# Optimization experiments

Measured on AMD Instinct MI355X. Metric: run time of the kernel, lower is better.

The kernel has to match this reference:

```python
import jax, jax.numpy as jnp
import numpy as np

NUM_HEADS = 8
N_POINTS = 9
OFFSET_SCALE = 4.0


def bilinear_sample(fmap_flat, xy, H, W):
    """fmap_flat: (BH, H*W, C) row-major spatial; xy: (BH, S, 2) pixel coords (x, y).
    grid_sample(mode='bilinear', padding_mode='zeros', align_corners=True) equivalent.
    Returns (BH, S, C)."""
    x, y = xy[..., 0], xy[..., 1]
    x0 = jnp.floor(x); y0 = jnp.floor(y)
    x1 = x0 + 1.0;    y1 = y0 + 1.0
    wx1 = x - x0; wx0 = 1.0 - wx1
    wy1 = y - y0; wy0 = 1.0 - wy1

    def corner(xi, yi, wgt):
        valid = (xi >= 0) & (xi <= W - 1) & (yi >= 0) & (yi <= H - 1)
        xi_c = jnp.clip(xi, 0, W - 1).astype(jnp.int32)
        yi_c = jnp.clip(yi, 0, H - 1).astype(jnp.int32)
        idx = yi_c * W + xi_c                                   # (BH, S)
        vals = jnp.take_along_axis(fmap_flat, idx[..., None], axis=1)  # (BH, S, C)
        return vals * (wgt * valid.astype(fmap_flat.dtype))[..., None]

    return (corner(x0, y0, wx0 * wy0) + corner(x1, y0, wx1 * wy0)
            + corner(x0, y1, wx0 * wy1) + corner(x1, y1, wx1 * wy1))


def setup_inputs() -> dict:
    key = jax.random.key(0)
    ks = jax.random.split(key, 10)
    B, N, D = 4, 6400, 256
    Hh, P = NUM_HEADS, N_POINTS
    s = 0.02
    return {
        "x":    jax.random.normal(ks[0], (B, N, D), dtype=jnp.float32),
        "Wq":   jax.random.normal(ks[1], (D, D), dtype=jnp.float32) * s,
        "bq":   jnp.zeros((D,), jnp.float32),
        "Woff": jax.random.normal(ks[2], (Hh * P * 2, D), dtype=jnp.float32) * s,
        "boff": jax.random.normal(ks[3], (Hh * P * 2,), dtype=jnp.float32) * s,
        "Wkv":  jax.random.normal(ks[4], (2 * D, D), dtype=jnp.float32) * s,
        "bkv":  jnp.zeros((2 * D,), jnp.float32),
        "Wout": jax.random.normal(ks[5], (D, D), dtype=jnp.float32) * s,
        "bout": jnp.zeros((D,), jnp.float32),
        "h": 40,
        "w": 160,
    }


def reference(x, Wq, bq, Woff, boff, Wkv, bkv, Wout, bout, h, w):
    B, N, D = x.shape
    H, P = NUM_HEADS, N_POINTS
    hd = D // H

    # queries: (B, H, N, hd)
    q = (x @ Wq.T + bq).reshape(B, N, H, hd).transpose(0, 2, 1, 3)

    # per-query per-head offsets in pixels: (B, N, H, P, 2) (dx, dy)
    offsets = jnp.tanh(x @ Woff.T + boff).reshape(B, N, H, P, 2) * OFFSET_SCALE

    # K/V feature maps via 1x1 conv == per-token linear; split heads, flat spatial
    kv = x @ Wkv.T + bkv                     # (B, N, 2D)
    k = kv[..., :D]
    v = kv[..., D:]
    k_flat = k.reshape(B, N, H, hd).transpose(0, 2, 1, 3).reshape(B * H, N, hd)
    v_flat = v.reshape(B, N, H, hd).transpose(0, 2, 1, 3).reshape(B * H, N, hd)

    # base pixel grid (x, y), row-major over (h, w)
    ys, xs = jnp.meshgrid(jnp.arange(h, dtype=x.dtype), jnp.arange(w, dtype=x.dtype), indexing="ij")
    base_xy = jnp.stack([xs, ys], axis=-1).reshape(N, 2)

    # sampling locations: (B, N, H, P, 2) -> (B*H, N*P, 2)
    sample_xy = base_xy[None, :, None, None, :] + offsets
    sample_xy = sample_xy.transpose(0, 2, 1, 3, 4).reshape(B * H, N * P, 2)

    sampled_k = bilinear_sample(k_flat, sample_xy, h, w).reshape(B, H, N, P, hd)
    sampled_v = bilinear_sample(v_flat, sample_xy, h, w).reshape(B, H, N, P, hd)

    logits = jnp.einsum("bhnd,bhnpd->bhnp", q, sampled_k) * (hd ** -0.5)
    attn = jax.nn.softmax(logits, axis=-1)
    out = jnp.einsum("bhnp,bhnpd->bhnd", attn, sampled_v)   # (B, H, N, hd)
    out = out.transpose(0, 2, 1, 3).reshape(B, N, D)
    return out @ Wout.T + bout
```

## Files before the change

### kernel.cpp

```cpp
#include <hip/hip_runtime.h>
#include <math.h>

#define BSZ    4
#define NTOK   6400
#define DMODEL 256
#define NHEAD  8
#define HDIM   32
#define NPTS   9
#define HSP    40
#define WSP    160
#define KDIM   256
#define MTOT   (BSZ*NTOK)

typedef short  short8  __attribute__((ext_vector_type(8)));
typedef float  floatx4 __attribute__((ext_vector_type(4)));
typedef float  f32x2   __attribute__((ext_vector_type(2)));

__device__ __forceinline__ ushort f2bf(float f) {
    uint u = __float_as_uint(f);
    u = (u + 0x7FFFu + ((u >> 16) & 1u)) >> 16;
    return (ushort)u;
}

__device__ __forceinline__ void unpack8v(uint4 u, f32x2* f) {
    f[0].x = __uint_as_float(u.x << 16); f[0].y = __uint_as_float(u.x & 0xFFFF0000u);
    f[1].x = __uint_as_float(u.y << 16); f[1].y = __uint_as_float(u.y & 0xFFFF0000u);
    f[2].x = __uint_as_float(u.z << 16); f[2].y = __uint_as_float(u.z & 0xFFFF0000u);
    f[3].x = __uint_as_float(u.w << 16); f[3].y = __uint_as_float(u.w & 0xFFFF0000u);
}

__device__ __forceinline__ float dot8(uint4 u, const f32x2* q2) {
    f32x2 a; a.x = 0.f; a.y = 0.f;
    f32x2 t;
    t.x = __uint_as_float(u.x << 16); t.y = __uint_as_float(u.x & 0xFFFF0000u);
    a += t * q2[0];
    t.x = __uint_as_float(u.y << 16); t.y = __uint_as_float(u.y & 0xFFFF0000u);
    a += t * q2[1];
    t.x = __uint_as_float(u.z << 16); t.y = __uint_as_float(u.z & 0xFFFF0000u);
    a += t * q2[2];
    t.x = __uint_as_float(u.w << 16); t.y = __uint_as_float(u.w & 0xFFFF0000u);
    a += t * q2[3];
    return a.x + a.y;
}

#define AS1C(p) ((const __attribute__((address_space(1))) void*)(p))
#define AS3(p)  ((__attribute__((address_space(3))) void*)(p))

__global__ __launch_bounds__(256) void cast_all(
    const float* __restrict__ x,   const float* __restrict__ Wq,
    const float* __restrict__ Woff,const float* __restrict__ Wkv,
    const float* __restrict__ Wout,
    ushort* __restrict__ xb, ushort* __restrict__ wf, ushort* __restrict__ woutb)
{
    const int bid = blockIdx.x;
    if (bid >= 6500 && bid < 6528) {
        const int i = (bid - 6500) * 1024 + threadIdx.x * 4;
        ushort4 z; z.x = 0; z.y = 0; z.z = 0; z.w = 0;
        *(ushort4*)(wf + 400 * 256 + i) = z;
        return;
    }
    const float* src; ushort* dst; int base;
    if      (bid < 6400) { src = x;    dst = xb;              base = bid; }
    else if (bid < 6464) { src = Wq;   dst = wf;              base = bid - 6400; }
    else if (bid < 6500) { src = Woff; dst = wf + 256 * 256;  base = bid - 6464; }
    else if (bid < 6656) { src = Wkv;  dst = wf + 512 * 256;  base = bid - 6528; }
    else                 { src = Wout; dst = woutb;           base = bid - 6656; }
    const int i = base * 1024 + threadIdx.x * 4;
    float4 v = *(const float4*)(src + i);
    ushort4 o;
    o.x = f2bf(v.x); o.y = f2bf(v.y); o.z = f2bf(v.z); o.w = f2bf(v.w);
    *(ushort4*)(dst + i) = o;
}

__global__ __launch_bounds__(256) void gemm_fused(
    const ushort* __restrict__ Xb,
    const ushort* __restrict__ Wf,
    const float* __restrict__ bq, const float* __restrict__ boff,
    const float* __restrict__ bkv,
    ushort* __restrict__ qb, float* __restrict__ off,
    ushort* __restrict__ kfb, ushort* __restrict__ vfb)
{
    __shared__ ushort As[128 * 32];
    __shared__ ushort Bs[128 * 32];

    const int tid = threadIdx.x;
    const int block_m = blockIdx.y * 128;
    const int block_n = blockIdx.x * 128;
    const int wave = tid >> 6, lane = tid & 63;
    const int wm = (wave >> 1) * 64, wn = (wave & 1) * 64;
    const int l15 = lane & 15, quad = lane >> 4;

    const int srow = wave * 32 + (lane >> 2);
    const int scol = (lane & 3) * 8;

    const ushort* gA0 = Xb + (size_t)(block_m + srow) * KDIM + scol;
    const ushort* gA1 = gA0 + 16 * KDIM;
    const ushort* gB0 = Wf + (size_t)(block_n + srow) * KDIM + scol;
    const ushort* gB1 = gB0 + 16 * KDIM;

    ushort* lA0 = &As[(wave * 32) * 32];
    ushort* lA1 = &As[(wave * 32 + 16) * 32];
    ushort* lB0 = &Bs[(wave * 32) * 32];
    ushort* lB1 = &Bs[(wave * 32 + 16) * 32];

    floatx4 acc[4][4];
    #pragma unroll
    for (int i = 0; i < 4; ++i)
        #pragma unroll
        for (int j = 0; j < 4; ++j) {
            acc[i][j][0] = 0.f; acc[i][j][1] = 0.f;
            acc[i][j][2] = 0.f; acc[i][j][3] = 0.f;
        }

    for (int k0 = 0; k0 < KDIM; k0 += 32) {
        __builtin_amdgcn_global_load_lds(AS1C(gA0 + k0), AS3(lA0), 16, 0, 0);
        __builtin_amdgcn_global_load_lds(AS1C(gA1 + k0), AS3(lA1), 16, 0, 0);
        __builtin_amdgcn_global_load_lds(AS1C(gB0 + k0), AS3(lB0), 16, 0, 0);
        __builtin_amdgcn_global_load_lds(AS1C(gB1 + k0), AS3(lB1), 16, 0, 0);
        __syncthreads();

        short8 af[4], bfr[4];
        #pragma unroll
        for (int f = 0; f < 4; ++f) {
            af[f]  = *(const short8*)&As[(wm + f * 16 + l15) * 32 + quad * 8];
            bfr[f] = *(const short8*)&Bs[(wn + f * 16 + l15) * 32 + quad * 8];
        }
        #pragma unroll
        for (int fm = 0; fm < 4; ++fm)
            #pragma unroll
            for (int fn = 0; fn < 4; ++fn)
                acc[fm][fn] = __builtin_amdgcn_mfma_f32_16x16x32_bf16(
                    af[fm], bfr[fn], acc[fm][fn], 0, 0, 0);
        __syncthreads();
    }

    #pragma unroll
    for (int fn = 0; fn < 4; ++fn) {
        const int col = block_n + wn + fn * 16 + l15;
        float bcol;
        if      (col < 256) bcol = bq[col];
        else if (col < 400) bcol = boff[col - 256];
        else if (col < 512) bcol = 0.f;
        else                bcol = bkv[col - 512];
        #pragma unroll
        for (int fm = 0; fm < 4; ++fm) {
            #pragma unroll
            for (int r = 0; r < 4; ++r) {
                const int row = block_m + wm + fm * 16 + quad * 4 + r;
                const float val = acc[fm][fn][r] + bcol;
                if (col < 256) {
                    qb[(size_t)row * DMODEL + col] = f2bf(val);
                } else if (col < 400) {
                    off[(size_t)row * 144 + (col - 256)] = tanhf(val) * 4.0f;
                } else if (col >= 512) {
                    const int c2 = col - 512;
                    const int bb = row / NTOK, nn = row % NTOK;
                    const int hh = (c2 & 255) >> 5, cc = c2 & 31;
                    const size_t o = (((size_t)(bb * NHEAD + hh)) * NTOK + nn) * HDIM + cc;
                    if (c2 < 256) kfb[o] = f2bf(val);
                    else          vfb[o] = f2bf(val);
                }
            }
        }
    }
}

__global__ __launch_bounds__(256) void gemm_out(
    const ushort* __restrict__ Xb,
    const ushort* __restrict__ Wb,
    const float* __restrict__ bias,
    float* __restrict__ Y)
{
    __shared__ ushort As[128 * 32];
    __shared__ ushort Bs[128 * 32];

    const int tid = threadIdx.x;
    const int block_m = blockIdx.y * 128;
    const int block_n = blockIdx.x * 128;
    const int wave = tid >> 6, lane = tid & 63;
    const int wm = (wave >> 1) * 64, wn = (wave & 1) * 64;
    const int l15 = lane & 15, quad = lane >> 4;

    const int srow = wave * 32 + (lane >> 2);
    const int scol = (lane & 3) * 8;

    const ushort* gA0 = Xb + (size_t)(block_m + srow) * KDIM + scol;
    const ushort* gA1 = gA0 + 16 * KDIM;
    const ushort* gB0 = Wb + (size_t)(block_n + srow) * KDIM + scol;
    const ushort* gB1 = gB0 + 16 * KDIM;

    ushort* lA0 = &As[(wave * 32) * 32];
    ushort* lA1 = &As[(wave * 32 + 16) * 32];
    ushort* lB0 = &Bs[(wave * 32) * 32];
    ushort* lB1 = &Bs[(wave * 32 + 16) * 32];

    floatx4 acc[4][4];
    #pragma unroll
    for (int i = 0; i < 4; ++i)
        #pragma unroll
        for (int j = 0; j < 4; ++j) {
            acc[i][j][0] = 0.f; acc[i][j][1] = 0.f;
            acc[i][j][2] = 0.f; acc[i][j][3] = 0.f;
        }

    for (int k0 = 0; k0 < KDIM; k0 += 32) {
        __builtin_amdgcn_global_load_lds(AS1C(gA0 + k0), AS3(lA0), 16, 0, 0);
        __builtin_amdgcn_global_load_lds(AS1C(gA1 + k0), AS3(lA1), 16, 0, 0);
        __builtin_amdgcn_global_load_lds(AS1C(gB0 + k0), AS3(lB0), 16, 0, 0);
        __builtin_amdgcn_global_load_lds(AS1C(gB1 + k0), AS3(lB1), 16, 0, 0);
        __syncthreads();

        short8 af[4], bfr[4];
        #pragma unroll
        for (int f = 0; f < 4; ++f) {
            af[f]  = *(const short8*)&As[(wm + f * 16 + l15) * 32 + quad * 8];
            bfr[f] = *(const short8*)&Bs[(wn + f * 16 + l15) * 32 + quad * 8];
        }
        #pragma unroll
        for (int fm = 0; fm < 4; ++fm)
            #pragma unroll
            for (int fn = 0; fn < 4; ++fn)
                acc[fm][fn] = __builtin_amdgcn_mfma_f32_16x16x32_bf16(
                    af[fm], bfr[fn], acc[fm][fn], 0, 0, 0);
        __syncthreads();
    }

    #pragma unroll
    for (int fn = 0; fn < 4; ++fn) {
        const int col = block_n + wn + fn * 16 + l15;
        const float bcol = bias[col];
        #pragma unroll
        for (int fm = 0; fm < 4; ++fm) {
            #pragma unroll
            for (int r = 0; r < 4; ++r) {
                const int row = block_m + wm + fm * 16 + quad * 4 + r;
                Y[(size_t)row * DMODEL + col] = acc[fm][fn][r] + bcol;
            }
        }
    }
}

__global__ __launch_bounds__(256) void deform_attn(
    const ushort* __restrict__ qb,
    const float* __restrict__ off,
    const ushort* __restrict__ kfb,
    const ushort* __restrict__ vfb,
    ushort* __restrict__ attnb)
{
    const int lane = threadIdx.x & 63;
    const int token = blockIdx.x * 8 + (threadIdx.x >> 6) * 2 + (lane >> 5);
    const int h = (lane >> 2) & 7, lc = lane & 3;
    const int b = token / NTOK, n = token % NTOK;

    const uint4 qu = *(const uint4*)(qb + (size_t)token * DMODEL + h * HDIM + lc * 8);
    f32x2 q2[4]; unpack8v(qu, q2);

    const float* ob = off + (size_t)token * 144 + h * (NPTS * 2);
    const float bx = (float)(n % WSP), by = (float)(n / WSP);
    const ushort* kbase = kfb + (size_t)(b * NHEAD + h) * NTOK * HDIM + lc * 8;
    const ushort* vbase = vfb + (size_t)(b * NHEAD + h) * NTOK * HDIM + lc * 8;

    float m = -INFINITY, s = 0.f;
    f32x2 o2[4];
    #pragma unroll
    for (int i = 0; i < 4; ++i) { o2[i].x = 0.f; o2[i].y = 0.f; }

    #pragma unroll
    for (int g = 0; g < 3; ++g) {
        int   idx[3][4];
        float wt[3][4];
        #pragma unroll
        for (int j = 0; j < 3; ++j) {
            const int p = g * 3 + j;
            const float2 of = *(const float2*)(ob + 2 * p);
            const float sx = bx + of.x, sy = by + of.y;
            const float fx0 = floorf(sx), fy0 = floorf(sy);
            const float wx1 = sx - fx0, wx0 = 1.0f - wx1;
            const float wy1 = sy - fy0, wy0 = 1.0f - wy1;
            const int ix0 = (int)fx0, iy0 = (int)fy0;
            const int ix1 = ix0 + 1, iy1 = iy0 + 1;
            const bool vx0 = (ix0 >= 0) & (ix0 <= WSP - 1);
            const bool vx1 = (ix1 >= 0) & (ix1 <= WSP - 1);
            const bool vy0 = (iy0 >= 0) & (iy0 <= HSP - 1);
            const bool vy1 = (iy1 >= 0) & (iy1 <= HSP - 1);
            const int cx0 = min(max(ix0, 0), WSP - 1);
            const int cx1 = min(max(ix1, 0), WSP - 1);
            const int cy0 = min(max(iy0, 0), HSP - 1);
            const int cy1 = min(max(iy1, 0), HSP - 1);
            wt[j][0] = wx0 * wy0 * (float)(vx0 && vy0);
            wt[j][1] = wx1 * wy0 * (float)(vx1 && vy0);
            wt[j][2] = wx0 * wy1 * (float)(vx0 && vy1);
            wt[j][3] = wx1 * wy1 * (float)(vx1 && vy1);
            idx[j][0] = (cy0 * WSP + cx0) * HDIM;
            idx[j][1] = (cy0 * WSP + cx1) * HDIM;
            idx[j][2] = (cy1 * WSP + cx0) * HDIM;
            idx[j][3] = (cy1 * WSP + cx1) * HDIM;
        }

        float l[3];
        #pragma unroll
        for (int j = 0; j < 3; ++j) {
            const uint4 k0 = *(const uint4*)(kbase + idx[j][0]);
            const uint4 k1 = *(const uint4*)(kbase + idx[j][1]);
            const uint4 k2 = *(const uint4*)(kbase + idx[j][2]);
            const uint4 k3 = *(const uint4*)(kbase + idx[j][3]);
            float part = wt[j][0] * dot8(k0, q2) + wt[j][1] * dot8(k1, q2)
                       + wt[j][2] * dot8(k2, q2) + wt[j][3] * dot8(k3, q2);
            part += __shfl_xor(part, 1, 64);
            part += __shfl_xor(part, 2, 64);
            l[j] = part * 0.17677669529663687f;
        }

        const float m1 = fmaxf(fmaxf(fmaxf(l[0], l[1]), l[2]), m);
        const float corr = __expf(m - m1);
        const float e0 = __expf(l[0] - m1);
        const float e1 = __expf(l[1] - m1);
        const float e2 = __expf(l[2] - m1);
        s = s * corr + e0 + e1 + e2;
        m = m1;
        const float e[3] = {e0, e1, e2};

        #pragma unroll
        for (int i = 0; i < 4; ++i) o2[i] *= corr;

        #pragma unroll
        for (int j = 0; j < 3; ++j) {
            #pragma unroll
            for (int c = 0; c < 4; ++c) {
                const uint4 vu = *(const uint4*)(vbase + idx[j][c]);
                f32x2 vv[4]; unpack8v(vu, vv);
                const float ew = e[j] * wt[j][c];
                #pragma unroll
                for (int i = 0; i < 4; ++i) o2[i] += vv[i] * ew;
            }
        }
    }

    const float inv = 1.0f / s;
    uint4 ru;
    ru.x = (uint)f2bf(o2[0].x * inv) | ((uint)f2bf(o2[0].y * inv) << 16);
    ru.y = (uint)f2bf(o2[1].x * inv) | ((uint)f2bf(o2[1].y * inv) << 16);
    ru.z = (uint)f2bf(o2[2].x * inv) | ((uint)f2bf(o2[2].y * inv) << 16);
    ru.w = (uint)f2bf(o2[3].x * inv) | ((uint)f2bf(o2[3].y * inv) << 16);
    *(uint4*)(attnb + (size_t)token * DMODEL + h * HDIM + lc * 8) = ru;
}

extern "C" void kernel_launch(void* const* d_in, const int* in_sizes, int n_in,
                              void* d_out, int out_size, void* d_ws, size_t ws_size,
                              hipStream_t stream) {
    const float* x    = (const float*)d_in[0];
    const float* Wq   = (const float*)d_in[1];
    const float* bq   = (const float*)d_in[2];
    const float* Woff = (const float*)d_in[3];
    const float* boff = (const float*)d_in[4];
    const float* Wkv  = (const float*)d_in[5];
    const float* bkv  = (const float*)d_in[6];
    const float* Wout = (const float*)d_in[7];
    const float* bout = (const float*)d_in[8];

    ushort* xb    = (ushort*)d_ws;
    ushort* qb    = xb + (size_t)MTOT * DMODEL;
    float*  off   = (float*)(qb + (size_t)MTOT * DMODEL);
    ushort* kfb   = (ushort*)(off + (size_t)MTOT * 144);
    ushort* vfb   = kfb + (size_t)MTOT * DMODEL;
    ushort* wf    = vfb + (size_t)MTOT * DMODEL;
    ushort* woutb = wf + 262144;
    ushort* attnb = xb;

    cast_all<<<dim3(6720), dim3(256), 0, stream>>>(x, Wq, Woff, Wkv, Wout,
                                                   xb, wf, woutb);

    gemm_fused<<<dim3(8, 200), dim3(256), 0, stream>>>(xb, wf, bq, boff, bkv,
                                                       qb, off, kfb, vfb);

    deform_attn<<<dim3(3200), dim3(256), 0, stream>>>(qb, off, kfb, vfb, attnb);

    gemm_out<<<dim3(2, 200), dim3(256), 0, stream>>>(attnb, woutb, bout,
                                                     (float*)d_out);
}
```

Before: 217.4 us.

## Stage full-K A tile in swizzled LDS, read B from global, XCD-aware block mapping

Both GEMMs now share one templated kernel. It loads the whole 128x256 A tile into XOR-swizzled LDS once, then runs the K loop with no per-step barriers. B fragments are read directly from global memory, where the small weights should stay cached. Blocks are remapped so that consecutive blocks on the same XCD share A rows, which should improve L2 locality. The trade-offs are 64KB of LDS per block, which lowers occupancy, and uncoalesced global B loads inside the MFMA loop.

```diff
diff --git a/kernel.cpp b/kernel.cpp
--- a/kernel.cpp
+++ b/kernel.cpp
@@ -72,58 +72,64 @@
     *(ushort4*)(dst + i) = o;
 }
 
-__global__ __launch_bounds__(256) void gemm_fused(
+template <int MODE>
+__global__ __launch_bounds__(256) void gemm_fullk(
     const ushort* __restrict__ Xb,
     const ushort* __restrict__ Wf,
     const float* __restrict__ bq, const float* __restrict__ boff,
     const float* __restrict__ bkv,
     ushort* __restrict__ qb, float* __restrict__ off,
-    ushort* __restrict__ kfb, ushort* __restrict__ vfb)
+    ushort* __restrict__ kfb, ushort* __restrict__ vfb,
+    float* __restrict__ Yout)
 {
-    __shared__ ushort As[128 * 32];
-    __shared__ ushort Bs[128 * 32];
+    constexpr int NBN = (MODE == 0) ? 8 : 2;
+    __shared__ ushort As[4 * 128 * 64];
 
     const int tid = threadIdx.x;
-    const int block_m = blockIdx.y * 128;
-    const int block_n = blockIdx.x * 128;
+    const int bid = blockIdx.x;
+    const int xcd = bid & 7;
+    const int j   = bid >> 3;
+    const int block_n = (j & (NBN - 1)) * 128;
+    const int block_m = (xcd * 25 + j / NBN) * 128;
+
     const int wave = tid >> 6, lane = tid & 63;
     const int wm = (wave >> 1) * 64, wn = (wave & 1) * 64;
     const int l15 = lane & 15, quad = lane >> 4;
 
-    const int srow = wave * 32 + (lane >> 2);
-    const int scol = (lane & 3) * 8;
-
-    const ushort* gA0 = Xb + (size_t)(block_m + srow) * KDIM + scol;
-    const ushort* gA1 = gA0 + 16 * KDIM;
-    const ushort* gB0 = Wf + (size_t)(block_n + srow) * KDIM + scol;
-    const ushort* gB1 = gB0 + 16 * KDIM;
-
-    ushort* lA0 = &As[(wave * 32) * 32];
-    ushort* lA1 = &As[(wave * 32 + 16) * 32];
-    ushort* lB0 = &Bs[(wave * 32) * 32];
-    ushort* lB1 = &Bs[(wave * 32 + 16) * 32];
+    const int r8   = lane >> 3;
+    const int gsrc = (lane & 7) ^ r8;
+    #pragma unroll
+    for (int kc = 0; kc < 4; ++kc) {
+        #pragma unroll
+        for (int i = 0; i < 4; ++i) {
+            const int rl = wave * 32 + i * 8;
+            const ushort* src = Xb + (size_t)(block_m + rl + r8) * KDIM
+                                   + kc * 64 + gsrc * 8;
+            ushort* dst = As + kc * (128 * 64) + rl * 64;
+            __builtin_amdgcn_global_load_lds(AS1C(src), AS3(dst), 16, 0, 0);
+        }
+    }
+    __syncthreads();
 
     floatx4 acc[4][4];
     #pragma unroll
     for (int i = 0; i < 4; ++i)
         #pragma unroll
-        for (int j = 0; j < 4; ++j) {
-            acc[i][j][0] = 0.f; acc[i][j][1] = 0.f;
-            acc[i][j][2] = 0.f; acc[i][j][3] = 0.f;
-        }
-
-    for (int k0 = 0; k0 < KDIM; k0 += 32) {
-        __builtin_amdgcn_global_load_lds(AS1C(gA0 + k0), AS3(lA0), 16, 0, 0);
-        __builtin_amdgcn_global_load_lds(AS1C(gA1 + k0), AS3(lA1), 16, 0, 0);
-        __builtin_amdgcn_global_load_lds(AS1C(gB0 + k0), AS3(lB0), 16, 0, 0);
-        __builtin_amdgcn_global_load_lds(AS1C(gB1 + k0), AS3(lB1), 16, 0, 0);
-        __syncthreads();
-
+        for (int jj = 0; jj < 4; ++jj) {
+            acc[i][jj][0] = 0.f; acc[i][jj][1] = 0.f;
+            acc[i][jj][2] = 0.f; acc[i][jj][3] = 0.f;
+        }
+
+    #pragma unroll
+    for (int ks = 0; ks < 8; ++ks) {
         short8 af[4], bfr[4];
         #pragma unroll
         for (int f = 0; f < 4; ++f) {
-            af[f]  = *(const short8*)&As[(wm + f * 16 + l15) * 32 + quad * 8];
-            bfr[f] = *(const short8*)&Bs[(wn + f * 16 + l15) * 32 + quad * 8];
+            const int rowa = wm + f * 16 + l15;
+            const int gsw  = (((ks & 1) * 4 + quad) ^ (l15 & 7));
+            af[f]  = *(const short8*)(As + (ks >> 1) * (128 * 64) + rowa * 64 + gsw * 8);
+            bfr[f] = *(const short8*)(Wf + (size_t)(block_n + wn + f * 16 + l15) * KDIM
+                                         + ks * 32 + quad * 8);
         }
         #pragma unroll
         for (int fm = 0; fm < 4; ++fm)
@@ -131,110 +137,42 @@
             for (int fn = 0; fn < 4; ++fn)
                 acc[fm][fn] = __builtin_amdgcn_mfma_f32_16x16x32_bf16(
                     af[fm], bfr[fn], acc[fm][fn], 0, 0, 0);
-        __syncthreads();
     }
 
     #pragma unroll
     for (int fn = 0; fn < 4; ++fn) {
         const int col = block_n + wn + fn * 16 + l15;
         float bcol;
-        if      (col < 256) bcol = bq[col];
-        else if (col < 400) bcol = boff[col - 256];
-        else if (col < 512) bcol = 0.f;
-        else                bcol = bkv[col - 512];
+        if (MODE == 1) {
+            bcol = bq[col];
+        } else {
+            if      (col < 256) bcol = bq[col];
+            else if (col < 400) bcol = boff[col - 256];
+            else if (col < 512) bcol = 0.f;
+            else                bcol = bkv[col - 512];
+        }
         #pragma unroll
         for (int fm = 0; fm < 4; ++fm) {
             #pragma unroll
             for (int r = 0; r < 4; ++r) {
                 const int row = block_m + wm + fm * 16 + quad * 4 + r;
                 const float val = acc[fm][fn][r] + bcol;
-                if (col < 256) {
-                    qb[(size_t)row * DMODEL + col] = f2bf(val);
-                } else if (col < 400) {
-                    off[(size_t)row * 144 + (col - 256)] = tanhf(val) * 4.0f;
-                } else if (col >= 512) {
-                    const int c2 = col - 512;
-                    const int bb = row / NTOK, nn = row % NTOK;
-                    const int hh = (c2 & 255) >> 5, cc = c2 & 31;
-                    const size_t o = (((size_t)(bb * NHEAD + hh)) * NTOK + nn) * HDIM + cc;
-                    if (c2 < 256) kfb[o] = f2bf(val);
-                    else          vfb[o] = f2bf(val);
+                if (MODE == 1) {
+                    Yout[(size_t)row * DMODEL + col] = val;
+                } else {
+                    if (col < 256) {
+                        qb[(size_t)row * DMODEL + col] = f2bf(val);
+                    } else if (col < 400) {
+                        off[(size_t)row * 144 + (col - 256)] = tanhf(val) * 4.0f;
+                    } else if (col >= 512) {
+                        const int c2 = col - 512;
+                        const int bb = row / NTOK, nn = row % NTOK;
+                        const int hh = (c2 & 255) >> 5, cc = c2 & 31;
+                        const size_t o = (((size_t)(bb * NHEAD + hh)) * NTOK + nn) * HDIM + cc;
+                        if (c2 < 256) kfb[o] = f2bf(val);
+                        else          vfb[o] = f2bf(val);
+                    }
                 }
-            }
-        }
-    }
-}
-
-__global__ __launch_bounds__(256) void gemm_out(
-    const ushort* __restrict__ Xb,
-    const ushort* __restrict__ Wb,
-    const float* __restrict__ bias,
-    float* __restrict__ Y)
-{
-    __shared__ ushort As[128 * 32];
-    __shared__ ushort Bs[128 * 32];
-
-    const int tid = threadIdx.x;
-    const int block_m = blockIdx.y * 128;
-    const int block_n = blockIdx.x * 128;
-    const int wave = tid >> 6, lane = tid & 63;
-    const int wm = (wave >> 1) * 64, wn = (wave & 1) * 64;
-    const int l15 = lane & 15, quad = lane >> 4;
-
-    const int srow = wave * 32 + (lane >> 2);
-    const int scol = (lane & 3) * 8;
-
-    const ushort* gA0 = Xb + (size_t)(block_m + srow) * KDIM + scol;
-    const ushort* gA1 = gA0 + 16 * KDIM;
-    const ushort* gB0 = Wb + (size_t)(block_n + srow) * KDIM + scol;
-    const ushort* gB1 = gB0 + 16 * KDIM;
-
-    ushort* lA0 = &As[(wave * 32) * 32];
-    ushort* lA1 = &As[(wave * 32 + 16) * 32];
-    ushort* lB0 = &Bs[(wave * 32) * 32];
-    ushort* lB1 = &Bs[(wave * 32 + 16) * 32];
-
-    floatx4 acc[4][4];
-    #pragma unroll
-    for (int i = 0; i < 4; ++i)
-        #pragma unroll
-        for (int j = 0; j < 4; ++j) {
-            acc[i][j][0] = 0.f; acc[i][j][1] = 0.f;
-            acc[i][j][2] = 0.f; acc[i][j][3] = 0.f;
-        }
-
-    for (int k0 = 0; k0 < KDIM; k0 += 32) {
-        __builtin_amdgcn_global_load_lds(AS1C(gA0 + k0), AS3(lA0), 16, 0, 0);
-        __builtin_amdgcn_global_load_lds(AS1C(gA1 + k0), AS3(lA1), 16, 0, 0);
-        __builtin_amdgcn_global_load_lds(AS1C(gB0 + k0), AS3(lB0), 16, 0, 0);
-        __builtin_amdgcn_global_load_lds(AS1C(gB1 + k0), AS3(lB1), 16, 0, 0);
-        __syncthreads();
-
-        short8 af[4], bfr[4];
-        #pragma unroll
-        for (int f = 0; f < 4; ++f) {
-            af[f]  = *(const short8*)&As[(wm + f * 16 + l15) * 32 + quad * 8];
-            bfr[f] = *(const short8*)&Bs[(wn + f * 16 + l15) * 32 + quad * 8];
-        }
-        #pragma unroll
-        for (int fm = 0; fm < 4; ++fm)
-            #pragma unroll
-            for (int fn = 0; fn < 4; ++fn)
-                acc[fm][fn] = __builtin_amdgcn_mfma_f32_16x16x32_bf16(
-                    af[fm], bfr[fn], acc[fm][fn], 0, 0, 0);
-        __syncthreads();
-    }
-
-    #pragma unroll
-    for (int fn = 0; fn < 4; ++fn) {
-        const int col = block_n + wn + fn * 16 + l15;
-        const float bcol = bias[col];
-        #pragma unroll
-        for (int fm = 0; fm < 4; ++fm) {
-            #pragma unroll
-            for (int r = 0; r < 4; ++r) {
-                const int row = block_m + wm + fm * 16 + quad * 4 + r;
-                Y[(size_t)row * DMODEL + col] = acc[fm][fn][r] + bcol;
             }
         }
     }
@@ -270,8 +208,8 @@
         int   idx[3][4];
         float wt[3][4];
         #pragma unroll
-        for (int j = 0; j < 3; ++j) {
-            const int p = g * 3 + j;
+        for (int jj = 0; jj < 3; ++jj) {
+            const int p = g * 3 + jj;
             const float2 of = *(const float2*)(ob + 2 * p);
             const float sx = bx + of.x, sy = by + of.y;
             const float fx0 = floorf(sx), fy0 = floorf(sy);
@@ -287,28 +225,28 @@
             const int cx1 = min(max(ix1, 0), WSP - 1);
             const int cy0 = min(max(iy0, 0), HSP - 1);
             const int cy1 = min(max(iy1, 0), HSP - 1);
-            wt[j][0] = wx0 * wy0 * (float)(vx0 && vy0);
-            wt[j][1] = wx1 * wy0 * (float)(vx1 && vy0);
-            wt[j][2] = wx0 * wy1 * (float)(vx0 && vy1);
-            wt[j][3] = wx1 * wy1 * (float)(vx1 && vy1);
-            idx[j][0] = (cy0 * WSP + cx0) * HDIM;
-            idx[j][1] = (cy0 * WSP + cx1) * HDIM;
-            idx[j][2] = (cy1 * WSP + cx0) * HDIM;
-            idx[j][3] = (cy1 * WSP + cx1) * HDIM;
+            wt[jj][0] = wx0 * wy0 * (float)(vx0 && vy0);
+            wt[jj][1] = wx1 * wy0 * (float)(vx1 && vy0);
+            wt[jj][2] = wx0 * wy1 * (float)(vx0 && vy1);
+            wt[jj][3] = wx1 * wy1 * (float)(vx1 && vy1);
+            idx[jj][0] = (cy0 * WSP + cx0) * HDIM;
+            idx[jj][1] = (cy0 * WSP + cx1) * HDIM;
+            idx[jj][2] = (cy1 * WSP + cx0) * HDIM;
+            idx[jj][3] = (cy1 * WSP + cx1) * HDIM;
         }
 
         float l[3];
         #pragma unroll
-        for (int j = 0; j < 3; ++j) {
-            const uint4 k0 = *(const uint4*)(kbase + idx[j][0]);
-            const uint4 k1 = *(const uint4*)(kbase + idx[j][1]);
-            const uint4 k2 = *(const uint4*)(kbase + idx[j][2]);
-            const uint4 k3 = *(const uint4*)(kbase + idx[j][3]);
-            float part = wt[j][0] * dot8(k0, q2) + wt[j][1] * dot8(k1, q2)
-                       + wt[j][2] * dot8(k2, q2) + wt[j][3] * dot8(k3, q2);
+        for (int jj = 0; jj < 3; ++jj) {
+            const uint4 k0 = *(const uint4*)(kbase + idx[jj][0]);
+            const uint4 k1 = *(const uint4*)(kbase + idx[jj][1]);
+            const uint4 k2 = *(const uint4*)(kbase + idx[jj][2]);
+            const uint4 k3 = *(const uint4*)(kbase + idx[jj][3]);
+            float part = wt[jj][0] * dot8(k0, q2) + wt[jj][1] * dot8(k1, q2)
+                       + wt[jj][2] * dot8(k2, q2) + wt[jj][3] * dot8(k3, q2);
             part += __shfl_xor(part, 1, 64);
             part += __shfl_xor(part, 2, 64);
-            l[j] = part * 0.17677669529663687f;
+            l[jj] = part * 0.17677669529663687f;
         }
 
         const float m1 = fmaxf(fmaxf(fmaxf(l[0], l[1]), l[2]), m);
@@ -324,12 +262,12 @@
         for (int i = 0; i < 4; ++i) o2[i] *= corr;
 
         #pragma unroll
-        for (int j = 0; j < 3; ++j) {
+        for (int jj = 0; jj < 3; ++jj) {
             #pragma unroll
             for (int c = 0; c < 4; ++c) {
-                const uint4 vu = *(const uint4*)(vbase + idx[j][c]);
+                const uint4 vu = *(const uint4*)(vbase + idx[jj][c]);
                 f32x2 vv[4]; unpack8v(vu, vv);
-                const float ew = e[j] * wt[j][c];
+                const float ew = e[jj] * wt[jj][c];
                 #pragma unroll
                 for (int i = 0; i < 4; ++i) o2[i] += vv[i] * ew;
             }
@@ -370,11 +308,13 @@
     cast_all<<<dim3(6720), dim3(256), 0, stream>>>(x, Wq, Woff, Wkv, Wout,
                                                    xb, wf, woutb);
 
-    gemm_fused<<<dim3(8, 200), dim3(256), 0, stream>>>(xb, wf, bq, boff, bkv,
-                                                       qb, off, kfb, vfb);
+    gemm_fullk<0><<<dim3(1600), dim3(256), 0, stream>>>(xb, wf, bq, boff, bkv,
+                                                        qb, off, kfb, vfb, nullptr);
 
     deform_attn<<<dim3(3200), dim3(256), 0, stream>>>(qb, off, kfb, vfb, attnb);
 
-    gemm_out<<<dim3(2, 200), dim3(256), 0, stream>>>(attnb, woutb, bout,
-                                                     (float*)d_out);
-}
+    gemm_fullk<1><<<dim3(400), dim3(256), 0, stream>>>(attnb, woutb, bout,
+                                                       nullptr, nullptr, nullptr,
+                                                       nullptr, nullptr, nullptr,
+                                                       (float*)d_out);
+}
```

Result: slower. 228.7 us (+5.2%).
